# Performance work log

Measured on AMD Instinct MI355X. Metric: run time of the kernel, lower is better.

Reference implementation:

```python
import jax, jax.numpy as jnp
import numpy as np
from jax import lax

V, E, H, T, S = 100000, 256, 512, 9, 4096
HH = H // 2
START, STOP = 7, 8
NEG = -10000.0


def setup_inputs() -> dict:
    key = jax.random.key(0)
    ks = jax.random.split(key, 16)
    def n(k, shape, scale=0.1):
        return jax.random.normal(k, shape, jnp.float32) * scale
    sentence = jax.random.randint(ks[0], (S,), 0, V)
    embed = n(ks[1], (V, E), 1.0)
    w_ih_f = n(ks[2], (4 * HH, E)); w_hh_f = n(ks[3], (4 * HH, HH))
    b_ih_f = n(ks[4], (4 * HH,));   b_hh_f = n(ks[5], (4 * HH,))
    w_ih_b = n(ks[6], (4 * HH, E)); w_hh_b = n(ks[7], (4 * HH, HH))
    b_ih_b = n(ks[8], (4 * HH,));   b_hh_b = n(ks[9], (4 * HH,))
    h0 = n(ks[10], (2, HH), 1.0)  # init_hidden: randn (2,1,HH), batch squeezed
    c0 = n(ks[11], (2, HH), 1.0)
    W_out = n(ks[12], (T, H)); b_out = n(ks[13], (T,))
    transitions = jax.random.normal(ks[14], (T, T), jnp.float32)
    transitions = transitions.at[START, :].set(NEG).at[:, STOP].set(NEG)
    return dict(sentence=sentence, embed=embed,
                w_ih_f=w_ih_f, w_hh_f=w_hh_f, b_ih_f=b_ih_f, b_hh_f=b_hh_f,
                w_ih_b=w_ih_b, w_hh_b=w_hh_b, b_ih_b=b_ih_b, b_hh_b=b_hh_b,
                h0=h0, c0=c0, W_out=W_out, b_out=b_out, transitions=transitions)


def _lstm_dir(x_gates, h0, c0, w_hh):
    # x_gates: [S, 4*HH] = x @ w_ih.T + b_ih + b_hh (precomputed input part)
    def step(carry, xg):
        h, c = carry
        g = xg + h @ w_hh.T
        i, f, gg, o = jnp.split(g, 4)  # torch gate order: i, f, g, o
        i = jax.nn.sigmoid(i); f = jax.nn.sigmoid(f)
        gg = jnp.tanh(gg);     o = jax.nn.sigmoid(o)
        c = f * c + i * gg
        h = o * jnp.tanh(c)
        return (h, c), h
    _, hs = lax.scan(step, (h0, c0), x_gates)
    return hs  # [S, HH]


def reference(sentence, embed, w_ih_f, w_hh_f, b_ih_f, b_hh_f,
              w_ih_b, w_hh_b, b_ih_b, b_hh_b, h0, c0, W_out, b_out, transitions):
    x = embed[sentence]  # [S, E]
    # bidirectional LSTM, batch=1
    hf = _lstm_dir(x @ w_ih_f.T + b_ih_f + b_hh_f, h0[0], c0[0], w_hh_f)
    hb = _lstm_dir((x @ w_ih_b.T + b_ih_b + b_hh_b)[::-1], h0[1], c0[1], w_hh_b)[::-1]
    lstm_out = jnp.concatenate([hf, hb], axis=-1)          # [S, H]
    frames = lstm_out @ W_out.T + b_out                     # [S, T] emission scores

    # Viterbi-style decode (faithful: alpha updated by logsumexp, backpointers by argmax)
    alpha0 = jnp.full((T,), NEG, jnp.float32).at[START].set(0.0)
    def vstep(alpha, frame):
        smat = alpha[:, None] + frame[None, :] + transitions  # [T, T]
        bp = jnp.argmax(smat, axis=0)
        return jax.nn.logsumexp(smat, axis=0), bp
    alpha, bps = lax.scan(vstep, alpha0, frames)            # bps: [S, T]

    final = alpha + transitions[:, STOP]                     # [T]
    best = jnp.argmax(final)
    score = jax.nn.logsumexp(final)

    # backtrack over bps[1:] in reverse
    def bstep(tag, bp):
        nt = bp[tag]
        return nt, nt
    _, path_rev = lax.scan(bstep, best, bps[1:][::-1])
    tag_seq = jnp.concatenate([path_rev[::-1], best[None]])  # [S]
    return score, tag_seq
```

## Files before the change

### kernel.cpp

```cpp
#include <hip/hip_runtime.h>
#include <hip/hip_bf16.h>

#define SEQ   4096
#define EMB   256
#define HHID  256
#define G4    1024
#define NT    9
#define TSTART 7
#define TSTOP  8
#define NEGV  (-10000.0f)
#define POISON 0xAAAAAAAAu

#define WS_XG_F   0u
#define WS_XG_B   16777216u
#define WS_HF     33554432u
#define WS_HB     37748736u
#define WS_FRAMES 41943040u

#define PIDX(c) ((((c) >> 5) * 36) + ((c) & 31))

__global__ __launch_bounds__(256) void xgate_kernel(
    const int* __restrict__ sentence, const float* __restrict__ embed,
    const float* __restrict__ w_ih_f, const float* __restrict__ b_ih_f,
    const float* __restrict__ b_hh_f,
    const float* __restrict__ w_ih_b, const float* __restrict__ b_ih_b,
    const float* __restrict__ b_hh_b,
    float* __restrict__ xg_f, float* __restrict__ xg_b)
{
    const int st  = blockIdx.x;
    const int dir = blockIdx.y;
    const float* w  = dir ? w_ih_b : w_ih_f;
    const float* bi = dir ? b_ih_b : b_ih_f;
    const float* bh = dir ? b_hh_b : b_hh_f;
    float* xg = dir ? xg_b : xg_f;
    const int t = threadIdx.x;

    __shared__ float x_t[EMB][16];
    for (int sl = 0; sl < 16; ++sl) {
        int s   = st * 16 + sl;
        int tok = sentence[s];
        x_t[t][sl] = embed[(size_t)tok * EMB + t];
    }
    __syncthreads();

    float acc[4][16];
    #pragma unroll
    for (int q = 0; q < 4; ++q)
        #pragma unroll
        for (int sl = 0; sl < 16; ++sl) acc[q][sl] = 0.f;

    const float4* wr0 = (const float4*)(w + (size_t)(t      ) * EMB);
    const float4* wr1 = (const float4*)(w + (size_t)(t + 256) * EMB);
    const float4* wr2 = (const float4*)(w + (size_t)(t + 512) * EMB);
    const float4* wr3 = (const float4*)(w + (size_t)(t + 768) * EMB);
    #pragma unroll 2
    for (int e4 = 0; e4 < EMB / 4; ++e4) {
        float4 w0 = wr0[e4], w1 = wr1[e4], w2 = wr2[e4], w3 = wr3[e4];
        #pragma unroll
        for (int k = 0; k < 4; ++k) {
            float f0 = (k == 0) ? w0.x : (k == 1) ? w0.y : (k == 2) ? w0.z : w0.w;
            float f1 = (k == 0) ? w1.x : (k == 1) ? w1.y : (k == 2) ? w1.z : w1.w;
            float f2 = (k == 0) ? w2.x : (k == 1) ? w2.y : (k == 2) ? w2.z : w2.w;
            float f3 = (k == 0) ? w3.x : (k == 1) ? w3.y : (k == 2) ? w3.z : w3.w;
            int e = e4 * 4 + k;
            #pragma unroll
            for (int sl = 0; sl < 16; ++sl) {
                float xv = x_t[e][sl];
                acc[0][sl] += f0 * xv;
                acc[1][sl] += f1 * xv;
                acc[2][sl] += f2 * xv;
                acc[3][sl] += f3 * xv;
            }
        }
    }

    float bb0 = bi[t      ] + bh[t      ];
    float bb1 = bi[t + 256] + bh[t + 256];
    float bb2 = bi[t + 512] + bh[t + 512];
    float bb3 = bi[t + 768] + bh[t + 768];
    for (int sl = 0; sl < 16; ++sl) {
        float4 val = make_float4(acc[0][sl] + bb0, acc[1][sl] + bb1,
                                 acc[2][sl] + bb2, acc[3][sl] + bb3);
        ((float4*)(xg + (size_t)(st * 16 + sl) * G4))[t] = val;
    }
}

__global__ __launch_bounds__(256, 1) void lstm_kernel(
    const float* __restrict__ xg_f, const float* __restrict__ xg_b,
    const float* __restrict__ w_hh_f, const float* __restrict__ w_hh_b,
    const float* __restrict__ h0, const float* __restrict__ c0,
    float* __restrict__ hf, float* __restrict__ hb)
{
    const int bx    = blockIdx.x;
    const int dir   = bx >> 3;
    const int slice = bx & 7;
    const int t     = threadIdx.x;
    const int cb    = t & 7;
    const int rb    = t >> 3;
    const int unit  = slice * 32 + rb;

    const float* xg   = dir ? xg_b  : xg_f;
    const float* w_hh = dir ? w_hh_b : w_hh_f;
    float* hout = dir ? hb : hf;

    __shared__ float buf[2][288];

    float wa[128];
    #pragma unroll
    for (int q = 0; q < 4; ++q) {
        #pragma unroll
        for (int j = 0; j < 32; ++j) {
            float tmp = w_hh[(size_t)(q * HHID + unit) * HHID + cb * 32 + j];
            asm volatile("v_accvgpr_write_b32 %0, %1"
                         : "=a"(wa[q * 32 + j]) : "v"(tmp));
        }
    }

    float c_reg = 0.f;
    if (cb == 0) c_reg = c0[dir * HHID + unit];

    const bool own = (t >= slice * 32) && (t < slice * 32 + 32);

    for (int n = 0; n < SEQ; ++n) {
        const int s = dir ? (SEQ - 1 - n) : n;

        float4 xgv = make_float4(0.f, 0.f, 0.f, 0.f);
        if (cb == 0) {
            xgv = *(const float4*)(xg + (size_t)s * G4 + 4u * unit);
        }

        if (n == 0) {
            buf[0][PIDX(t)] = h0[dir * HHID + t];
        } else if (!own) {
            const int sp = dir ? (s + 1) : (s - 1);
            const unsigned int* src =
                (const unsigned int*)(hout + (size_t)sp * HHID) + t;
            unsigned v = __hip_atomic_load(src, __ATOMIC_RELAXED,
                                           __HIP_MEMORY_SCOPE_AGENT);
            if (v == POISON) {
                unsigned q0, q1, q2, q3;
                q0 = __hip_atomic_load(src, __ATOMIC_RELAXED,
                                       __HIP_MEMORY_SCOPE_AGENT);
                __builtin_amdgcn_s_sleep(2);
                q1 = __hip_atomic_load(src, __ATOMIC_RELAXED,
                                       __HIP_MEMORY_SCOPE_AGENT);
                __builtin_amdgcn_s_sleep(2);
                q2 = __hip_atomic_load(src, __ATOMIC_RELAXED,
                                       __HIP_MEMORY_SCOPE_AGENT);
                __builtin_amdgcn_s_sleep(2);
                q3 = __hip_atomic_load(src, __ATOMIC_RELAXED,
                                       __HIP_MEMORY_SCOPE_AGENT);
                for (;;) {
                    if (q0 != POISON) { v = q0; break; }
                    q0 = __hip_atomic_load(src, __ATOMIC_RELAXED,
                                           __HIP_MEMORY_SCOPE_AGENT);
                    if (q1 != POISON) { v = q1; break; }
                    q1 = __hip_atomic_load(src, __ATOMIC_RELAXED,
                                           __HIP_MEMORY_SCOPE_AGENT);
                    if (q2 != POISON) { v = q2; break; }
                    q2 = __hip_atomic_load(src, __ATOMIC_RELAXED,
                                           __HIP_MEMORY_SCOPE_AGENT);
                    if (q3 != POISON) { v = q3; break; }
                    q3 = __hip_atomic_load(src, __ATOMIC_RELAXED,
                                           __HIP_MEMORY_SCOPE_AGENT);
                }
            }
            buf[n & 1][PIDX(t)] = __uint_as_float(v);
        }
        __syncthreads();

        float a0 = 0.f, a1 = 0.f, a2 = 0.f, a3 = 0.f;
        const float4* h4 = (const float4*)(&buf[n & 1][cb * 36]);
        #pragma unroll
        for (int j4 = 0; j4 < 8; ++j4) {
            float4 hv = h4[j4];
            #pragma unroll
            for (int k = 0; k < 4; ++k) {
                float hk = (k == 0) ? hv.x : (k == 1) ? hv.y
                         : (k == 2) ? hv.z : hv.w;
                float w0, w1, w2, w3;
                asm volatile("v_accvgpr_read_b32 %0, %1"
                             : "=v"(w0) : "a"(wa[0 * 32 + j4 * 4 + k]));
                asm volatile("v_accvgpr_read_b32 %0, %1"
                             : "=v"(w1) : "a"(wa[1 * 32 + j4 * 4 + k]));
                asm volatile("v_accvgpr_read_b32 %0, %1"
                             : "=v"(w2) : "a"(wa[2 * 32 + j4 * 4 + k]));
                asm volatile("v_accvgpr_read_b32 %0, %1"
                             : "=v"(w3) : "a"(wa[3 * 32 + j4 * 4 + k]));
                a0 += w0 * hk;
                a1 += w1 * hk;
                a2 += w2 * hk;
                a3 += w3 * hk;
            }
        }

        #pragma unroll
        for (int m = 1; m <= 4; m <<= 1) {
            a0 += __shfl_xor(a0, m);
            a1 += __shfl_xor(a1, m);
            a2 += __shfl_xor(a2, m);
            a3 += __shfl_xor(a3, m);
        }

        if (cb == 0) {
            float gi = a0 + xgv.x;
            float gf = a1 + xgv.y;
            float gg = a2 + xgv.z;
            float go = a3 + xgv.w;
            float iv = 1.f / (1.f + __expf(-gi));
            float fv = 1.f / (1.f + __expf(-gf));
            float gv = 1.f - 2.f / (__expf(2.f * gg) + 1.f);
            float ov = 1.f / (1.f + __expf(-go));
            float c  = fv * c_reg + iv * gv;
            c_reg = c;
            float h  = ov * (1.f - 2.f / (__expf(2.f * c) + 1.f));
            unsigned int* dst =
                (unsigned int*)(hout + (size_t)s * HHID) + unit;
            __hip_atomic_store(dst, __float_as_uint(h), __ATOMIC_RELAXED,
                               __HIP_MEMORY_SCOPE_AGENT);
            buf[(n + 1) & 1][PIDX(unit)] = h;
        }
    }
}

__global__ __launch_bounds__(256) void frames_kernel(
    const float* __restrict__ hf, const float* __restrict__ hb,
    const float* __restrict__ W_out, const float* __restrict__ b_out,
    float* __restrict__ frames)
{
    int o = blockIdx.x * 256 + threadIdx.x;
    if (o >= SEQ * NT) return;
    int s = o / NT;
    int j = o - s * NT;
    const float4* a0 = (const float4*)(hf + (size_t)s * HHID);
    const float4* a1 = (const float4*)(hb + (size_t)s * HHID);
    const float4* w0 = (const float4*)(W_out + (size_t)j * 512);
    const float4* w1 = w0 + 64;
    float acc = 0.f;
    #pragma unroll 8
    for (int i = 0; i < 64; ++i) {
        float4 a = a0[i], b = w0[i];
        acc += a.x * b.x + a.y * b.y + a.z * b.z + a.w * b.w;
        float4 c = a1[i], d = w1[i];
        acc += c.x * d.x + c.y * d.y + c.z * d.z + c.w * d.w;
    }
    frames[o] = acc + b_out[j];
}

__global__ __launch_bounds__(64) void crf_kernel(
    const float* __restrict__ frames, const float* __restrict__ trans,
    float* __restrict__ dout)
{
    __shared__ float fr[512 * NT];
    __shared__ unsigned char bpl[SEQ * NT];
    const int t = threadIdx.x;
    const int tc = (t < NT) ? t : 0;

    float trow[NT];
    #pragma unroll
    for (int i = 0; i < NT; ++i) trow[i] = 0.f;
    if (t < NT) {
        #pragma unroll
        for (int i = 0; i < NT; ++i) trow[i] = trans[i * NT + t];
    }
    float alpha = (t == TSTART) ? 0.f : NEGV;

    for (int chunk = 0; chunk < 8; ++chunk) {
        for (int idx = t; idx < 512 * NT; idx += 64)
            fr[idx] = frames[chunk * 512 * NT + idx];
        __syncthreads();

        for (int sl = 0; sl < 512; ++sl) {
            const int s = chunk * 512 + sl;
            float v[NT];
            #pragma unroll
            for (int i = 0; i < NT; ++i)
                v[i] = __shfl(alpha, i) + trow[i];
            float mx = v[0];
            int   am = 0;
            #pragma unroll
            for (int i = 1; i < NT; ++i)
                if (v[i] > mx) { mx = v[i]; am = i; }
            float sum = 0.f;
            #pragma unroll
            for (int i = 0; i < NT; ++i) sum += __expf(v[i] - mx);
            float anew = fr[sl * NT + tc] + mx + __logf(sum);
            if (t < NT) {
                bpl[s * NT + t] = (unsigned char)am;
                alpha = anew;
            }
        }
        __syncthreads();
    }

    float fin = NEGV;
    if (t < NT) fin = alpha + trans[t * NT + TSTOP];
    float f[NT];
    #pragma unroll
    for (int j = 0; j < NT; ++j) f[j] = __shfl(fin, j);

    if (t == 0) {
        float mx = f[0];
        int best = 0;
        #pragma unroll
        for (int j = 1; j < NT; ++j)
            if (f[j] > mx) { mx = f[j]; best = j; }
        float sum = 0.f;
        #pragma unroll
        for (int j = 0; j < NT; ++j) sum += __expf(f[j] - mx);
        dout[0] = mx + __logf(sum);

        int cur = best;
        dout[1 + SEQ - 1] = (float)cur;
        for (int s = SEQ - 2; s >= 0; --s) {
            cur = bpl[(s + 1) * NT + cur];
            dout[1 + s] = (float)cur;
        }
    }
}

extern "C" void kernel_launch(void* const* d_in, const int* in_sizes, int n_in,
                              void* d_out, int out_size, void* d_ws, size_t ws_size,
                              hipStream_t stream)
{
    const int*   sentence = (const int*)  d_in[0];
    const float* embed    = (const float*)d_in[1];
    const float* w_ih_f   = (const float*)d_in[2];
    const float* w_hh_f   = (const float*)d_in[3];
    const float* b_ih_f   = (const float*)d_in[4];
    const float* b_hh_f   = (const float*)d_in[5];
    const float* w_ih_b   = (const float*)d_in[6];
    const float* w_hh_b   = (const float*)d_in[7];
    const float* b_ih_b   = (const float*)d_in[8];
    const float* b_hh_b   = (const float*)d_in[9];
    const float* h0       = (const float*)d_in[10];
    const float* c0       = (const float*)d_in[11];
    const float* W_out    = (const float*)d_in[12];
    const float* b_out    = (const float*)d_in[13];
    const float* trans    = (const float*)d_in[14];

    float* out = (float*)d_out;
    char*  ws  = (char*)d_ws;

    float* xg_f   = (float*)(ws + WS_XG_F);
    float* xg_b   = (float*)(ws + WS_XG_B);
    float* hf     = (float*)(ws + WS_HF);
    float* hb     = (float*)(ws + WS_HB);
    float* frames = (float*)(ws + WS_FRAMES);

    hipMemsetAsync(hf, 0xAA, 2u * SEQ * HHID * sizeof(float), stream);

    xgate_kernel<<<dim3(256, 2), 256, 0, stream>>>(
        sentence, embed, w_ih_f, b_ih_f, b_hh_f, w_ih_b, b_ih_b, b_hh_b,
        xg_f, xg_b);

    lstm_kernel<<<16, 256, 0, stream>>>(
        xg_f, xg_b, w_hh_f, w_hh_b, h0, c0, hf, hb);

    frames_kernel<<<(SEQ * NT + 255) / 256, 256, 0, stream>>>(
        hf, hb, W_out, b_out, frames);

    crf_kernel<<<1, 64, 0, stream>>>(frames, trans, out);
}
```

Before: 9.914 ms.

## Pin LSTM recurrence blocks to one XCC and use sc0 loads for polling

Launches 1024 blocks and uses the hardware XCC id register plus an atomic ticket so the 16 working LSTM blocks all land on XCC 0, where they share an L2 and cross-block h exchange avoids the cross-die path. Polling switches to inline-asm global loads with the sc0 cache bit, with an occasional atomicOr fallback, and stores are issued both atomically and with sc0. This aims to cut the latency of the per-timestep cross-block handoff. In exchange it adds launch overhead for many empty blocks, borrows the frames buffer as control counters, and depends on undocumented cache-coherence behaviour of sc0 across CUs.

```diff
diff --git a/kernel.cpp b/kernel.cpp
--- a/kernel.cpp
+++ b/kernel.cpp
@@ -19,6 +19,22 @@
 
 #define PIDX(c) ((((c) >> 5) * 36) + ((c) & 31))
 
+#define XCC_HWREG ((31u << 11) | 20u)
+
+static __device__ __forceinline__ unsigned load_sc0(const unsigned* p)
+{
+    unsigned v;
+    asm volatile("global_load_dword %0, %1, off sc0\n\t"
+                 "s_waitcnt vmcnt(0)"
+                 : "=&v"(v) : "v"(p) : "memory");
+    return v;
+}
+static __device__ __forceinline__ void store_sc0(unsigned* p, unsigned v)
+{
+    asm volatile("global_store_dword %0, %1, off sc0"
+                 :: "v"(p), "v"(v) : "memory");
+}
+
 __global__ __launch_bounds__(256) void xgate_kernel(
     const int* __restrict__ sentence, const float* __restrict__ embed,
     const float* __restrict__ w_ih_f, const float* __restrict__ b_ih_f,
@@ -89,9 +105,24 @@
     const float* __restrict__ xg_f, const float* __restrict__ xg_b,
     const float* __restrict__ w_hh_f, const float* __restrict__ w_hh_b,
     const float* __restrict__ h0, const float* __restrict__ c0,
-    float* __restrict__ hf, float* __restrict__ hb)
-{
-    const int bx    = blockIdx.x;
+    float* __restrict__ hf, float* __restrict__ hb,
+    int* __restrict__ ctl)
+{
+    __shared__ int s_slot;
+    if (threadIdx.x == 0) {
+        unsigned xcc = __builtin_amdgcn_s_getreg(XCC_HWREG) & 0xFu;
+        int ticket = atomicAdd(&ctl[2], 1);
+        int slot = -1;
+        if (xcc == 0 || ticket >= 1008) {
+            int sl = atomicAdd(&ctl[1], 1);
+            if (sl < 16) slot = sl;
+        }
+        s_slot = slot;
+    }
+    __syncthreads();
+    const int bx = s_slot;
+    if (bx < 0) return;
+
     const int dir   = bx >> 3;
     const int slice = bx & 7;
     const int t     = threadIdx.x;
@@ -133,37 +164,14 @@
             buf[0][PIDX(t)] = h0[dir * HHID + t];
         } else if (!own) {
             const int sp = dir ? (s + 1) : (s - 1);
-            const unsigned int* src =
-                (const unsigned int*)(hout + (size_t)sp * HHID) + t;
-            unsigned v = __hip_atomic_load(src, __ATOMIC_RELAXED,
-                                           __HIP_MEMORY_SCOPE_AGENT);
-            if (v == POISON) {
-                unsigned q0, q1, q2, q3;
-                q0 = __hip_atomic_load(src, __ATOMIC_RELAXED,
-                                       __HIP_MEMORY_SCOPE_AGENT);
-                __builtin_amdgcn_s_sleep(2);
-                q1 = __hip_atomic_load(src, __ATOMIC_RELAXED,
-                                       __HIP_MEMORY_SCOPE_AGENT);
-                __builtin_amdgcn_s_sleep(2);
-                q2 = __hip_atomic_load(src, __ATOMIC_RELAXED,
-                                       __HIP_MEMORY_SCOPE_AGENT);
-                __builtin_amdgcn_s_sleep(2);
-                q3 = __hip_atomic_load(src, __ATOMIC_RELAXED,
-                                       __HIP_MEMORY_SCOPE_AGENT);
-                for (;;) {
-                    if (q0 != POISON) { v = q0; break; }
-                    q0 = __hip_atomic_load(src, __ATOMIC_RELAXED,
-                                           __HIP_MEMORY_SCOPE_AGENT);
-                    if (q1 != POISON) { v = q1; break; }
-                    q1 = __hip_atomic_load(src, __ATOMIC_RELAXED,
-                                           __HIP_MEMORY_SCOPE_AGENT);
-                    if (q2 != POISON) { v = q2; break; }
-                    q2 = __hip_atomic_load(src, __ATOMIC_RELAXED,
-                                           __HIP_MEMORY_SCOPE_AGENT);
-                    if (q3 != POISON) { v = q3; break; }
-                    q3 = __hip_atomic_load(src, __ATOMIC_RELAXED,
-                                           __HIP_MEMORY_SCOPE_AGENT);
-                }
+            unsigned* src = (unsigned*)(hout + (size_t)sp * HHID) + t;
+            unsigned v = load_sc0(src);
+            int spin = 0;
+            while (v == POISON) {
+                if ((++spin & 7) == 0)
+                    v = atomicOr(src, 0u);
+                else
+                    v = load_sc0(src);
             }
             buf[n & 1][PIDX(t)] = __uint_as_float(v);
         }
@@ -214,10 +222,11 @@
             float c  = fv * c_reg + iv * gv;
             c_reg = c;
             float h  = ov * (1.f - 2.f / (__expf(2.f * c) + 1.f));
-            unsigned int* dst =
-                (unsigned int*)(hout + (size_t)s * HHID) + unit;
-            __hip_atomic_store(dst, __float_as_uint(h), __ATOMIC_RELAXED,
+            unsigned hu = __float_as_uint(h);
+            unsigned* dst = (unsigned*)(hout + (size_t)s * HHID) + unit;
+            __hip_atomic_store(dst, hu, __ATOMIC_RELAXED,
                                __HIP_MEMORY_SCOPE_AGENT);
+            store_sc0(dst, hu);
             buf[(n + 1) & 1][PIDX(unit)] = h;
         }
     }
@@ -349,13 +358,14 @@
     float* frames = (float*)(ws + WS_FRAMES);
 
     hipMemsetAsync(hf, 0xAA, 2u * SEQ * HHID * sizeof(float), stream);
+    hipMemsetAsync(frames, 0, 64, stream);
 
     xgate_kernel<<<dim3(256, 2), 256, 0, stream>>>(
         sentence, embed, w_ih_f, b_ih_f, b_hh_f, w_ih_b, b_ih_b, b_hh_b,
         xg_f, xg_b);
 
-    lstm_kernel<<<16, 256, 0, stream>>>(
-        xg_f, xg_b, w_hh_f, w_hh_b, h0, c0, hf, hb);
+    lstm_kernel<<<1024, 256, 0, stream>>>(
+        xg_f, xg_b, w_hh_f, w_hh_b, h0, c0, hf, hb, (int*)frames);
 
     frames_kernel<<<(SEQ * NT + 255) / 256, 256, 0, stream>>>(
         hf, hb, W_out, b_out, frames);
```

Result: slower. 14.33 ms (+44.6%).

## Parallelize Viterbi backtrack across wavefront lanes via composed backpointer maps

Applied to the files above, without the earlier changes.

Replaces the single-thread serial backtrack over 4096 steps with a lane-parallel scheme. Each of 64 lanes packs 64 steps of backpointer tables into nibble-encoded registers and composes them into one segment map. A 64-step shuffle scan propagates tags across segments, then each lane expands its own segment in parallel. It also vectorizes the frame load into shared memory and computes the argmax through a max tree plus an equality scan, which keeps first-index tie-breaking. In exchange it uses many registers (128 unsigned arrays per lane), which may cause spilling.

```diff
diff --git a/kernel.cpp b/kernel.cpp
--- a/kernel.cpp
+++ b/kernel.cpp
@@ -247,6 +247,13 @@
     frames[o] = acc + b_out[j];
 }
 
+__device__ __forceinline__ unsigned nib_ext(unsigned lo, unsigned hi,
+                                            unsigned idx)
+{
+    unsigned a = (lo >> ((4u * idx) & 31u)) & 15u;
+    return (idx < 8u) ? a : (hi & 15u);
+}
+
 __global__ __launch_bounds__(64) void crf_kernel(
     const float* __restrict__ frames, const float* __restrict__ trans,
     float* __restrict__ dout)
@@ -266,8 +273,10 @@
     float alpha = (t == TSTART) ? 0.f : NEGV;
 
     for (int chunk = 0; chunk < 8; ++chunk) {
-        for (int idx = t; idx < 512 * NT; idx += 64)
-            fr[idx] = frames[chunk * 512 * NT + idx];
+        const float4* src4 = (const float4*)(frames + chunk * 512 * NT);
+        float4* dst4 = (float4*)fr;
+        for (int idx = t; idx < 512 * NT / 4; idx += 64)
+            dst4[idx] = src4[idx];
         __syncthreads();
 
         for (int sl = 0; sl < 512; ++sl) {
@@ -276,11 +285,14 @@
             #pragma unroll
             for (int i = 0; i < NT; ++i)
                 v[i] = __shfl(alpha, i) + trow[i];
-            float mx = v[0];
-            int   am = 0;
+            float m01 = fmaxf(v[0], v[1]), m23 = fmaxf(v[2], v[3]);
+            float m45 = fmaxf(v[4], v[5]), m67 = fmaxf(v[6], v[7]);
+            float m03 = fmaxf(m01, m23),   m47 = fmaxf(m45, m67);
+            float mx  = fmaxf(fmaxf(m03, m47), v[8]);
+            int am = 8;
             #pragma unroll
-            for (int i = 1; i < NT; ++i)
-                if (v[i] > mx) { mx = v[i]; am = i; }
+            for (int i = 7; i >= 0; --i)
+                if (v[i] == mx) am = i;
             float sum = 0.f;
             #pragma unroll
             for (int i = 0; i < NT; ++i) sum += __expf(v[i] - mx);
@@ -299,23 +311,63 @@
     #pragma unroll
     for (int j = 0; j < NT; ++j) f[j] = __shfl(fin, j);
 
-    if (t == 0) {
-        float mx = f[0];
-        int best = 0;
-        #pragma unroll
-        for (int j = 1; j < NT; ++j)
-            if (f[j] > mx) { mx = f[j]; best = j; }
-        float sum = 0.f;
-        #pragma unroll
-        for (int j = 0; j < NT; ++j) sum += __expf(f[j] - mx);
-        dout[0] = mx + __logf(sum);
-
-        int cur = best;
-        dout[1 + SEQ - 1] = (float)cur;
-        for (int s = SEQ - 2; s >= 0; --s) {
-            cur = bpl[(s + 1) * NT + cur];
-            dout[1 + s] = (float)cur;
-        }
+    float mx2 = f[0];
+    int best = 0;
+    #pragma unroll
+    for (int j = 1; j < NT; ++j)
+        if (f[j] > mx2) { mx2 = f[j]; best = j; }
+    float sum2 = 0.f;
+    #pragma unroll
+    for (int j = 0; j < NT; ++j) sum2 += __expf(f[j] - mx2);
+    if (t == 0) dout[0] = mx2 + __logf(sum2);
+
+    unsigned rlo[64], rhi[64];
+    {
+        const int base_u = t * 64 + 1;
+        #pragma unroll
+        for (int i = 0; i < 64; ++i) {
+            unsigned lo, hi;
+            if (t == 63 && i == 63) {
+                lo = 0x76543210u; hi = 8u;
+            } else {
+                const int u = base_u + i;
+                lo = 0;
+                #pragma unroll
+                for (int k = 0; k < 8; ++k)
+                    lo |= ((unsigned)bpl[u * NT + k]) << (4 * k);
+                hi = (unsigned)bpl[u * NT + 8];
+            }
+            rlo[i] = lo; rhi[i] = hi;
+        }
+    }
+
+    unsigned gm[NT];
+    #pragma unroll
+    for (int k = 0; k < NT; ++k) gm[k] = (unsigned)k;
+    #pragma unroll
+    for (int i = 63; i >= 0; --i) {
+        #pragma unroll
+        for (int k = 0; k < NT; ++k)
+            gm[k] = nib_ext(rlo[i], rhi[i], gm[k]);
+    }
+    unsigned Glo = 0, Ghi = gm[8] & 15u;
+    #pragma unroll
+    for (int k = 0; k < 8; ++k) Glo |= gm[k] << (4 * k);
+
+    int cur = best;
+    int E   = best;
+    for (int lx = 63; lx >= 0; --lx) {
+        unsigned glo = __shfl(Glo, lx);
+        unsigned ghi = __shfl(Ghi, lx);
+        if (t == lx) E = cur;
+        cur = (int)nib_ext(glo, ghi, (unsigned)cur);
+    }
+
+    unsigned tg = (unsigned)E;
+    #pragma unroll
+    for (int i = 63; i >= 0; --i) {
+        tg = nib_ext(rlo[i], rhi[i], tg);
+        dout[1 + t * 64 + i] = (float)tg;
     }
 }
 
```

Measured after the change: 9.781 ms. About the same (-1.3%).
